# Kernel tuning notes

Hardware: AMD Instinct MI355X
Metric: run time of the kernel (lower is better)

Reference implementation:

```python
import jax, jax.numpy as jnp
import numpy as np
import math

EMBED_DIM = 1024
WINDOW = 512


def setup_inputs() -> dict:
    key = jax.random.key(0)
    k_x, k_mb, k_wg, k_bg = jax.random.split(key, 4)
    x = jax.random.normal(k_x, (4, 4096, EMBED_DIM), dtype=jnp.float32)
    memory_bank = jax.random.normal(k_mb, (WINDOW, EMBED_DIM), dtype=jnp.float32)
    # memory_gate: nn.Linear(embed_dim, embed_dim)
    lim = 1.0 / math.sqrt(EMBED_DIM)
    gate_w = jax.random.uniform(k_wg, (EMBED_DIM, EMBED_DIM), jnp.float32, -lim, lim)
    gate_b = jax.random.uniform(k_bg, (EMBED_DIM,), jnp.float32, -lim, lim)
    return {"x": x, "memory_bank": memory_bank, "gate_w": gate_w, "gate_b": gate_b}


def reference(x, memory_bank, gate_w, gate_b):
    d = x.shape[-1]
    # attention scores over fixed memory bank: [B, S, W]
    scores = jnp.einsum("bsd,wd->bsw", x, memory_bank) / jnp.sqrt(jnp.asarray(d, x.dtype))
    attn = jax.nn.softmax(scores, axis=-1)
    retrieved = jnp.einsum("bsw,wd->bsd", attn, memory_bank)
    gate = jax.nn.sigmoid(jnp.einsum("bsd,ed->bse", x, gate_w) + gate_b)
    return gate * x + (1.0 - gate) * retrieved
```

## Files before the change

kernel.cpp:

```cpp
#include <hip/hip_runtime.h>
#include <hip/hip_bf16.h>

#define EMBED 1024
#define WINDOW 512
#define NROWS 16384

typedef __attribute__((ext_vector_type(4))) float f32x4;
typedef __bf16 bf16x8 __attribute__((ext_vector_type(8)));

#define GLDS(g, l)                                                        \
  __builtin_amdgcn_global_load_lds(                                       \
      (const __attribute__((address_space(1))) void*)(const void*)(g),    \
      (__attribute__((address_space(3))) void*)(void*)(l), 16, 0, 0)

__global__ __launch_bounds__(256) void cast_bf16_kernel(
    const float* __restrict__ in, __bf16* __restrict__ out, int n8) {
  int i = blockIdx.x * blockDim.x + threadIdx.x;
  if (i >= n8) return;
  const f32x4* p = (const f32x4*)(in + (size_t)i * 8);
  f32x4 a = p[0], b = p[1];
  bf16x8 o = {(__bf16)a[0], (__bf16)a[1], (__bf16)a[2], (__bf16)a[3],
              (__bf16)b[0], (__bf16)b[1], (__bf16)b[2], (__bf16)b[3]};
  *(bf16x8*)(out + (size_t)i * 8) = o;
}

__global__ __launch_bounds__(256) void transpose_mb_kernel(
    const float* __restrict__ mb, __bf16* __restrict__ mbt) {
  int idx = blockIdx.x * blockDim.x + threadIdx.x;
  int w = idx >> 10, d = idx & 1023;
  mbt[(size_t)d * WINDOW + w] = (__bf16)mb[idx];
}

__global__ __launch_bounds__(256) void softmax_kernel(__bf16* __restrict__ s1) {
  const int row = blockIdx.x * 4 + (threadIdx.x >> 6);
  const int lane = threadIdx.x & 63;
  __bf16* p = s1 + (size_t)row * WINDOW + lane * 8;
  bf16x8 v = *(const bf16x8*)p;
  float f[8];
  float mx = -1e30f;
#pragma unroll
  for (int j = 0; j < 8; ++j) {
    f[j] = (float)v[j] * 0.03125f;
    mx = fmaxf(mx, f[j]);
  }
#pragma unroll
  for (int off = 1; off < 64; off <<= 1) mx = fmaxf(mx, __shfl_xor(mx, off));
  float s = 0.f;
#pragma unroll
  for (int j = 0; j < 8; ++j) {
    f[j] = __expf(f[j] - mx);
    s += f[j];
  }
#pragma unroll
  for (int off = 1; off < 64; off <<= 1) s += __shfl_xor(s, off);
  const float inv = 1.0f / s;
  bf16x8 o;
#pragma unroll
  for (int j = 0; j < 8; ++j) o[j] = (__bf16)(f[j] * inv);
  *(bf16x8*)p = o;
}

#define SLOADFRAGS(cb, kk)                                                    \
  {                                                                           \
    const __bf16* As_ = &ldsA[cb][(warp_m * 64 + fr) * 64];                   \
    const __bf16* Bs_ = &ldsB[cb][(warp_n * 64 + fr) * 64];                   \
    const int pg_ = (((kk)*4 + fq) ^ (fr & 7)) * 8;                           \
    _Pragma("unroll") for (int m = 0; m < 4; ++m)                             \
        af[m] = *(const bf16x8*)(As_ + m * 16 * 64 + pg_);                    \
    _Pragma("unroll") for (int n = 0; n < 4; ++n)                             \
        bfv[n] = *(const bf16x8*)(Bs_ + n * 16 * 64 + pg_);                   \
  }

#define SMFMA16(ACC)                                                          \
  {                                                                           \
    __builtin_amdgcn_s_barrier();                                             \
    asm volatile("s_waitcnt lgkmcnt(0)" ::: "memory");                        \
    __builtin_amdgcn_s_setprio(1);                                            \
    _Pragma("unroll") for (int m = 0; m < 4; ++m)                             \
        _Pragma("unroll") for (int n = 0; n < 4; ++n)                         \
            ACC[m][n] = __builtin_amdgcn_mfma_f32_16x16x32_bf16(              \
                af[m], bfv[n], ACC[m][n], 0, 0, 0);                           \
    __builtin_amdgcn_s_setprio(0);                                            \
    __builtin_amdgcn_s_barrier();                                             \
  }

__global__ __launch_bounds__(512, 2) void gemm_scores_kernel(
    const __bf16* __restrict__ xb, const __bf16* __restrict__ mbb,
    __bf16* __restrict__ s1) {
  __shared__ __align__(16) __bf16 ldsA[3][256 * 64];
  __shared__ __align__(16) __bf16 ldsB[3][128 * 64];
  const int tid = threadIdx.x;
  const int lane = tid & 63;
  const int wave = tid >> 6;
  const int bid = blockIdx.x;
  const int xcd = bid & 7;
  const int idx = bid >> 3;
  const int bm = xcd * 8 + (idx & 7);
  const int bn = idx >> 3;
  const int row0 = bm * 256;
  const int col0 = bn * 128;
  const int warp_m = wave >> 1;
  const int warp_n = wave & 1;
  const int srow = lane >> 3;
  const int sgc = (lane & 7) ^ srow;
  const int wv32 = wave * 32;
  const int wv16 = wave * 16;
  const int fr = lane & 15;
  const int fq = lane >> 4;

  const __bf16* aS = xb + (size_t)(row0 + wv32 + srow) * EMBED + sgc * 8;
  const __bf16* bS = mbb + (size_t)(col0 + wv16 + srow) * EMBED + sgc * 8;

#define STAGE_S1(vt, buf)                                                     \
  {                                                                           \
    const int k0_ = (vt)*64;                                                  \
    _Pragma("unroll") for (int c = 0; c < 2; ++c)                             \
        GLDS(aS + (size_t)c * 8 * EMBED + k0_, &ldsA[buf][(wv32 + c * 8) * 64]); \
    GLDS(bS + k0_, &ldsB[buf][wv16 * 64]);                                    \
  }
#define STAGE_S2(vt, buf)                                                     \
  {                                                                           \
    const int k0_ = (vt)*64;                                                  \
    _Pragma("unroll") for (int c = 2; c < 4; ++c)                             \
        GLDS(aS + (size_t)c * 8 * EMBED + k0_, &ldsA[buf][(wv32 + c * 8) * 64]); \
    GLDS(bS + (size_t)8 * EMBED + k0_, &ldsB[buf][(wv16 + 8) * 64]);          \
  }

  f32x4 acc[4][4];
#pragma unroll
  for (int m = 0; m < 4; ++m)
#pragma unroll
    for (int n = 0; n < 4; ++n) acc[m][n] = (f32x4){0.f, 0.f, 0.f, 0.f};
  bf16x8 af[4], bfv[4];

  STAGE_S1(0, 0); STAGE_S2(0, 0);
  STAGE_S1(1, 1); STAGE_S2(1, 1);
  asm volatile("s_waitcnt vmcnt(6)" ::: "memory");
  __builtin_amdgcn_s_barrier();

  const int NT = 16;
  for (int vt = 0; vt < NT; ++vt) {
    const int cb = vt % 3;
    const int nb = (vt + 2) % 3;
    SLOADFRAGS(cb, 0);
    if (vt + 2 < NT) STAGE_S1(vt + 2, nb);
    SMFMA16(acc);
    SLOADFRAGS(cb, 1);
    if (vt + 2 < NT) STAGE_S2(vt + 2, nb);
    if (vt < NT - 2) {
      asm volatile("s_waitcnt vmcnt(6)" ::: "memory");
    } else if (vt == NT - 2) {
      asm volatile("s_waitcnt vmcnt(0)" ::: "memory");
    }
    SMFMA16(acc);
  }
#undef STAGE_S1
#undef STAGE_S2

#pragma unroll
  for (int n = 0; n < 4; ++n) {
    const int col = col0 + warp_n * 64 + n * 16 + fr;
#pragma unroll
    for (int m = 0; m < 4; ++m)
#pragma unroll
      for (int j = 0; j < 4; ++j) {
        const int row = row0 + warp_m * 64 + m * 16 + fq * 4 + j;
        s1[(size_t)row * WINDOW + col] = (__bf16)acc[m][n][j];
      }
  }
}

__global__ __launch_bounds__(256, 2) void dual_fused128_kernel(
    const __bf16* __restrict__ s1, const __bf16* __restrict__ xb,
    const __bf16* __restrict__ mbt, const __bf16* __restrict__ gwb,
    const float* __restrict__ gb, float* __restrict__ out) {
  __shared__ __align__(16) __bf16 ldsA[2][128 * 64];
  __shared__ __align__(16) __bf16 ldsB[2][128 * 64];
  const int tid = threadIdx.x, lane = tid & 63, wave = tid >> 6;
  const int bid = blockIdx.x;
  const int xcd = bid & 7;
  const int g = bid >> 3;
  const int bm = xcd * 16 + (g & 15);
  const int bn = g >> 4;
  const int row0 = bm * 128, col0 = bn * 128;
  const int warp_m = wave >> 1, warp_n = wave & 1;
  const int fr = lane & 15, fq = lane >> 4;
  const int srow = lane >> 3;
  const int sgc = (lane & 7) ^ srow;
  const int wv32 = wave * 32;

  const __bf16* aR = s1 + (size_t)(row0 + wv32 + srow) * WINDOW + sgc * 8;
  const __bf16* bR = mbt + (size_t)(col0 + wv32 + srow) * WINDOW + sgc * 8;
  const __bf16* aG = xb + (size_t)(row0 + wv32 + srow) * EMBED + sgc * 8;
  const __bf16* bG = gwb + (size_t)(col0 + wv32 + srow) * EMBED + sgc * 8;

#define STG(vt, buf)                                                          \
  {                                                                           \
    if ((vt) < 8) {                                                           \
      const int k0_ = (vt)*64;                                                \
      _Pragma("unroll") for (int c = 0; c < 4; ++c)                           \
          GLDS(aR + (size_t)c * 8 * WINDOW + k0_,                             \
               &ldsA[buf][(wv32 + c * 8) * 64]);                              \
      _Pragma("unroll") for (int c = 0; c < 4; ++c)                           \
          GLDS(bR + (size_t)c * 8 * WINDOW + k0_,                             \
               &ldsB[buf][(wv32 + c * 8) * 64]);                              \
    } else {                                                                  \
      const int k0_ = ((vt)-8) * 64;                                          \
      _Pragma("unroll") for (int c = 0; c < 4; ++c)                           \
          GLDS(aG + (size_t)c * 8 * EMBED + k0_,                              \
               &ldsA[buf][(wv32 + c * 8) * 64]);                              \
      _Pragma("unroll") for (int c = 0; c < 4; ++c)                           \
          GLDS(bG + (size_t)c * 8 * EMBED + k0_,                              \
               &ldsB[buf][(wv32 + c * 8) * 64]);                              \
    }                                                                         \
  }

#define BARF                                                                  \
  {                                                                           \
    asm volatile("" ::: "memory");                                            \
    __builtin_amdgcn_s_barrier();                                             \
    asm volatile("" ::: "memory");                                            \
  }

#define COMPUTE(ACC, cur)                                                     \
  {                                                                           \
    const __bf16* As_ = &ldsA[cur][(warp_m * 64 + fr) * 64];                  \
    const __bf16* Bs_ = &ldsB[cur][(warp_n * 64 + fr) * 64];                  \
    _Pragma("unroll") for (int kk = 0; kk < 2; ++kk) {                        \
      const int pg_ = ((kk * 4 + fq) ^ (fr & 7)) * 8;                         \
      bf16x8 af[4], bfv[4];                                                   \
      _Pragma("unroll") for (int m = 0; m < 4; ++m)                           \
          af[m] = *(const bf16x8*)(As_ + m * 16 * 64 + pg_);                  \
      _Pragma("unroll") for (int n = 0; n < 4; ++n)                           \
          bfv[n] = *(const bf16x8*)(Bs_ + n * 16 * 64 + pg_);                 \
      __builtin_amdgcn_s_setprio(1);                                          \
      _Pragma("unroll") for (int m = 0; m < 4; ++m)                           \
          _Pragma("unroll") for (int n = 0; n < 4; ++n)                       \
              ACC[m][n] = __builtin_amdgcn_mfma_f32_16x16x32_bf16(            \
                  af[m], bfv[n], ACC[m][n], 0, 0, 0);                         \
      __builtin_amdgcn_s_setprio(0);                                          \
    }                                                                         \
  }

  f32x4 accr[4][4], accg[4][4];
#pragma unroll
  for (int m = 0; m < 4; ++m)
#pragma unroll
    for (int n = 0; n < 4; ++n) {
      accr[m][n] = (f32x4){0.f, 0.f, 0.f, 0.f};
      accg[m][n] = (f32x4){0.f, 0.f, 0.f, 0.f};
    }

  STG(0, 0);
  for (int vt = 0; vt < 8; ++vt) {
    const int cur = vt & 1;
    STG(vt + 1, cur ^ 1);
    asm volatile("s_waitcnt vmcnt(8)" ::: "memory");
    BARF;
    COMPUTE(accr, cur);
    BARF;
  }
  for (int vt = 8; vt < 24; ++vt) {
    const int cur = vt & 1;
    if (vt + 1 < 24) {
      STG(vt + 1, cur ^ 1);
      asm volatile("s_waitcnt vmcnt(8)" ::: "memory");
    } else {
      asm volatile("s_waitcnt vmcnt(0)" ::: "memory");
    }
    BARF;
    COMPUTE(accg, cur);
    BARF;
  }
#undef STG
#undef COMPUTE
#undef BARF

#pragma unroll
  for (int n = 0; n < 4; ++n) {
    const int col = col0 + warp_n * 64 + n * 16 + fr;
    const float bias = gb[col];
#pragma unroll
    for (int m = 0; m < 4; ++m) {
#pragma unroll
      for (int j = 0; j < 4; ++j) {
        const int row = row0 + warp_m * 64 + m * 16 + fq * 4 + j;
        const size_t o = (size_t)row * EMBED + col;
        const float gt = 1.0f / (1.0f + __expf(-(accg[m][n][j] + bias)));
        const float xv = (float)xb[o];
        out[o] = gt * xv + (1.0f - gt) * accr[m][n][j];
      }
    }
  }
}

extern "C" void kernel_launch(void* const* d_in, const int* in_sizes, int n_in,
                              void* d_out, int out_size, void* d_ws,
                              size_t ws_size, hipStream_t stream) {
  const float* x = (const float*)d_in[0];
  const float* mb = (const float*)d_in[1];
  const float* gw = (const float*)d_in[2];
  const float* gb = (const float*)d_in[3];
  float* out = (float*)d_out;

  char* ws = (char*)d_ws;
  __bf16* xb = (__bf16*)(ws);
  __bf16* mbb = (__bf16*)(ws + 33554432);
  __bf16* mbt = (__bf16*)(ws + 34603008);
  __bf16* gwb = (__bf16*)(ws + 35651584);
  __bf16* s1 = (__bf16*)(ws + 37748736);

  cast_bf16_kernel<<<8192, 256, 0, stream>>>(x, xb, 2097152);
  cast_bf16_kernel<<<256, 256, 0, stream>>>(mb, mbb, 65536);
  cast_bf16_kernel<<<512, 256, 0, stream>>>(gw, gwb, 131072);
  transpose_mb_kernel<<<2048, 256, 0, stream>>>(mb, mbt);
  gemm_scores_kernel<<<256, 512, 0, stream>>>(xb, mbb, s1);
  softmax_kernel<<<4096, 256, 0, stream>>>(s1);
  dual_fused128_kernel<<<1024, 256, 0, stream>>>(s1, xb, mbt, gwb, gb, out);
}
```

Measured before the change: 124.4 us.

## Enlarge dual GEMM tile to 256x256 and pack retrieved accumulator to bf16

The fused retrieval+gate GEMM moves from 128x128 tiles with 256 threads to 256x256 tiles with 512 threads, launching 256 blocks instead of 1024. Each wave now computes a 128x64 sub-tile, reusing B fragments across two A halves to raise arithmetic intensity and cut global/LDS traffic per FLOP. To keep register pressure manageable, the retrieved-value accumulator is packed to bf16 before the gate GEMM starts. This adds rounding to the retrieved term and raises LDS use per block (128KB), which lowers occupancy to about one block per CU.

```diff
diff --git a/kernel.cpp b/kernel.cpp
--- a/kernel.cpp
+++ b/kernel.cpp
@@ -170,20 +170,19 @@
   }
 }
 
-__global__ __launch_bounds__(256, 2) void dual_fused128_kernel(
+__global__ __launch_bounds__(512, 2) void dual_fused256_kernel(
     const __bf16* __restrict__ s1, const __bf16* __restrict__ xb,
     const __bf16* __restrict__ mbt, const __bf16* __restrict__ gwb,
     const float* __restrict__ gb, float* __restrict__ out) {
-  __shared__ __align__(16) __bf16 ldsA[2][128 * 64];
-  __shared__ __align__(16) __bf16 ldsB[2][128 * 64];
+  __shared__ __align__(16) __bf16 ldsA[2][256 * 64];
+  __shared__ __align__(16) __bf16 ldsB[2][256 * 64];
   const int tid = threadIdx.x, lane = tid & 63, wave = tid >> 6;
   const int bid = blockIdx.x;
-  const int xcd = bid & 7;
-  const int g = bid >> 3;
-  const int bm = xcd * 16 + (g & 15);
-  const int bn = g >> 4;
-  const int row0 = bm * 128, col0 = bn * 128;
-  const int warp_m = wave >> 1, warp_n = wave & 1;
+  const int bm = (bid & 7) * 8 + ((bid >> 3) & 7);
+  const int bn = bid >> 6;
+  const int row0 = bm * 256, col0 = bn * 256;
+  const int warp_m = wave >> 2;
+  const int warp_n = wave & 3;
   const int fr = lane & 15, fq = lane >> 4;
   const int srow = lane >> 3;
   const int sgc = (lane & 7) ^ srow;
@@ -224,32 +223,37 @@
 
 #define COMPUTE(ACC, cur)                                                     \
   {                                                                           \
-    const __bf16* As_ = &ldsA[cur][(warp_m * 64 + fr) * 64];                  \
+    const __bf16* As_ = &ldsA[cur][(warp_m * 128 + fr) * 64];                 \
     const __bf16* Bs_ = &ldsB[cur][(warp_n * 64 + fr) * 64];                  \
     _Pragma("unroll") for (int kk = 0; kk < 2; ++kk) {                        \
       const int pg_ = ((kk * 4 + fq) ^ (fr & 7)) * 8;                         \
       bf16x8 af[4], bfv[4];                                                   \
+      _Pragma("unroll") for (int n = 0; n < 4; ++n)                           \
+          bfv[n] = *(const bf16x8*)(Bs_ + n * 16 * 64 + pg_);                 \
       _Pragma("unroll") for (int m = 0; m < 4; ++m)                           \
           af[m] = *(const bf16x8*)(As_ + m * 16 * 64 + pg_);                  \
-      _Pragma("unroll") for (int n = 0; n < 4; ++n)                           \
-          bfv[n] = *(const bf16x8*)(Bs_ + n * 16 * 64 + pg_);                 \
       __builtin_amdgcn_s_setprio(1);                                          \
       _Pragma("unroll") for (int m = 0; m < 4; ++m)                           \
           _Pragma("unroll") for (int n = 0; n < 4; ++n)                       \
               ACC[m][n] = __builtin_amdgcn_mfma_f32_16x16x32_bf16(            \
                   af[m], bfv[n], ACC[m][n], 0, 0, 0);                         \
       __builtin_amdgcn_s_setprio(0);                                          \
+      _Pragma("unroll") for (int m = 0; m < 4; ++m)                           \
+          af[m] = *(const bf16x8*)(As_ + (64 + m * 16) * 64 + pg_);           \
+      __builtin_amdgcn_s_setprio(1);                                          \
+      _Pragma("unroll") for (int m = 0; m < 4; ++m)                           \
+          _Pragma("unroll") for (int n = 0; n < 4; ++n)                       \
+              ACC[4 + m][n] = __builtin_amdgcn_mfma_f32_16x16x32_bf16(        \
+                  af[m], bfv[n], ACC[4 + m][n], 0, 0, 0);                     \
+      __builtin_amdgcn_s_setprio(0);                                          \
     }                                                                         \
   }
 
-  f32x4 accr[4][4], accg[4][4];
-#pragma unroll
-  for (int m = 0; m < 4; ++m)
-#pragma unroll
-    for (int n = 0; n < 4; ++n) {
-      accr[m][n] = (f32x4){0.f, 0.f, 0.f, 0.f};
-      accg[m][n] = (f32x4){0.f, 0.f, 0.f, 0.f};
-    }
+  f32x4 accr[8][4];
+#pragma unroll
+  for (int m = 0; m < 8; ++m)
+#pragma unroll
+    for (int n = 0; n < 4; ++n) accr[m][n] = (f32x4){0.f, 0.f, 0.f, 0.f};
 
   STG(0, 0);
   for (int vt = 0; vt < 8; ++vt) {
@@ -260,6 +264,26 @@
     COMPUTE(accr, cur);
     BARF;
   }
+
+  unsigned pk[8][4][2];
+#pragma unroll
+  for (int m = 0; m < 8; ++m)
+#pragma unroll
+    for (int n = 0; n < 4; ++n) {
+      unsigned b0 = (unsigned)__builtin_bit_cast(unsigned short, (__bf16)accr[m][n][0]);
+      unsigned b1 = (unsigned)__builtin_bit_cast(unsigned short, (__bf16)accr[m][n][1]);
+      unsigned b2 = (unsigned)__builtin_bit_cast(unsigned short, (__bf16)accr[m][n][2]);
+      unsigned b3 = (unsigned)__builtin_bit_cast(unsigned short, (__bf16)accr[m][n][3]);
+      pk[m][n][0] = (b1 << 16) | b0;
+      pk[m][n][1] = (b3 << 16) | b2;
+    }
+
+  f32x4 accg[8][4];
+#pragma unroll
+  for (int m = 0; m < 8; ++m)
+#pragma unroll
+    for (int n = 0; n < 4; ++n) accg[m][n] = (f32x4){0.f, 0.f, 0.f, 0.f};
+
   for (int vt = 8; vt < 24; ++vt) {
     const int cur = vt & 1;
     if (vt + 1 < 24) {
@@ -281,14 +305,19 @@
     const int col = col0 + warp_n * 64 + n * 16 + fr;
     const float bias = gb[col];
 #pragma unroll
-    for (int m = 0; m < 4; ++m) {
+    for (int m = 0; m < 8; ++m) {
+      float rv[4];
+      rv[0] = __builtin_bit_cast(float, pk[m][n][0] << 16);
+      rv[1] = __builtin_bit_cast(float, pk[m][n][0] & 0xffff0000u);
+      rv[2] = __builtin_bit_cast(float, pk[m][n][1] << 16);
+      rv[3] = __builtin_bit_cast(float, pk[m][n][1] & 0xffff0000u);
 #pragma unroll
       for (int j = 0; j < 4; ++j) {
-        const int row = row0 + warp_m * 64 + m * 16 + fq * 4 + j;
+        const int row = row0 + warp_m * 128 + m * 16 + fq * 4 + j;
         const size_t o = (size_t)row * EMBED + col;
-        const float gt = 1.0f / (1.0f + __expf(-(accg[m][n][j] + bias)));
+        const float g = 1.0f / (1.0f + __expf(-(accg[m][n][j] + bias)));
         const float xv = (float)xb[o];
-        out[o] = gt * xv + (1.0f - gt) * accr[m][n][j];
+        out[o] = g * xv + (1.0f - g) * rv[j];
       }
     }
   }
@@ -316,5 +345,5 @@
   transpose_mb_kernel<<<2048, 256, 0, stream>>>(mb, mbt);
   gemm_scores_kernel<<<256, 512, 0, stream>>>(xb, mbb, s1);
   softmax_kernel<<<4096, 256, 0, stream>>>(s1);
-  dual_fused128_kernel<<<1024, 256, 0, stream>>>(s1, xb, mbt, gwb, gb, out);
-}
+  dual_fused256_kernel<<<256, 512, 0, stream>>>(s1, xb, mbt, gwb, gb, out);
+}
```

Measured after the change: 165.6 us. +33.1%, slower.

## Switch dual GEMM to BK=32 with four-stage LDS pipeline

Applied to the files above, without the earlier changes.

Halves the K tile of the fused retrieval/gate GEMM from 64 to 32 and moves from double buffering to a 4-slot ring with three tiles in flight. The LDS swizzle and load mapping are changed to match the narrower tile. The goal is to hide more global-load latency behind MFMA work. In exchange there are twice as many barrier pairs per K, less MFMA work per barrier, and an explicit lgkmcnt wait before the MFMAs.

```diff
diff --git a/kernel.cpp b/kernel.cpp
--- a/kernel.cpp
+++ b/kernel.cpp
@@ -170,12 +170,12 @@
   }
 }
 
-__global__ __launch_bounds__(256, 2) void dual_fused128_kernel(
+__global__ __launch_bounds__(256, 2) void dual_bk32_kernel(
     const __bf16* __restrict__ s1, const __bf16* __restrict__ xb,
     const __bf16* __restrict__ mbt, const __bf16* __restrict__ gwb,
     const float* __restrict__ gb, float* __restrict__ out) {
-  __shared__ __align__(16) __bf16 ldsA[2][128 * 64];
-  __shared__ __align__(16) __bf16 ldsB[2][128 * 64];
+  __shared__ __align__(16) __bf16 ldsA[4][128 * 32];
+  __shared__ __align__(16) __bf16 ldsB[4][128 * 32];
   const int tid = threadIdx.x, lane = tid & 63, wave = tid >> 6;
   const int bid = blockIdx.x;
   const int xcd = bid & 7;
@@ -185,8 +185,8 @@
   const int row0 = bm * 128, col0 = bn * 128;
   const int warp_m = wave >> 1, warp_n = wave & 1;
   const int fr = lane & 15, fq = lane >> 4;
-  const int srow = lane >> 3;
-  const int sgc = (lane & 7) ^ srow;
+  const int srow = lane >> 2;
+  const int sgc = (lane & 3) ^ (srow & 3);
   const int wv32 = wave * 32;
 
   const __bf16* aR = s1 + (size_t)(row0 + wv32 + srow) * WINDOW + sgc * 8;
@@ -194,24 +194,20 @@
   const __bf16* aG = xb + (size_t)(row0 + wv32 + srow) * EMBED + sgc * 8;
   const __bf16* bG = gwb + (size_t)(col0 + wv32 + srow) * EMBED + sgc * 8;
 
-#define STG(vt, buf)                                                          \
-  {                                                                           \
-    if ((vt) < 8) {                                                           \
-      const int k0_ = (vt)*64;                                                \
-      _Pragma("unroll") for (int c = 0; c < 4; ++c)                           \
-          GLDS(aR + (size_t)c * 8 * WINDOW + k0_,                             \
-               &ldsA[buf][(wv32 + c * 8) * 64]);                              \
-      _Pragma("unroll") for (int c = 0; c < 4; ++c)                           \
-          GLDS(bR + (size_t)c * 8 * WINDOW + k0_,                             \
-               &ldsB[buf][(wv32 + c * 8) * 64]);                              \
+#define STG(vt, slot)                                                         \
+  {                                                                           \
+    if ((vt) < 16) {                                                          \
+      const int k0_ = (vt)*32;                                                \
+      GLDS(aR + k0_, &ldsA[slot][wv32 * 32]);                                 \
+      GLDS(aR + (size_t)16 * WINDOW + k0_, &ldsA[slot][(wv32 + 16) * 32]);    \
+      GLDS(bR + k0_, &ldsB[slot][wv32 * 32]);                                 \
+      GLDS(bR + (size_t)16 * WINDOW + k0_, &ldsB[slot][(wv32 + 16) * 32]);    \
     } else {                                                                  \
-      const int k0_ = ((vt)-8) * 64;                                          \
-      _Pragma("unroll") for (int c = 0; c < 4; ++c)                           \
-          GLDS(aG + (size_t)c * 8 * EMBED + k0_,                              \
-               &ldsA[buf][(wv32 + c * 8) * 64]);                              \
-      _Pragma("unroll") for (int c = 0; c < 4; ++c)                           \
-          GLDS(bG + (size_t)c * 8 * EMBED + k0_,                              \
-               &ldsB[buf][(wv32 + c * 8) * 64]);                              \
+      const int k0_ = ((vt)-16) * 32;                                         \
+      GLDS(aG + k0_, &ldsA[slot][wv32 * 32]);                                 \
+      GLDS(aG + (size_t)16 * EMBED + k0_, &ldsA[slot][(wv32 + 16) * 32]);     \
+      GLDS(bG + k0_, &ldsB[slot][wv32 * 32]);                                 \
+      GLDS(bG + (size_t)16 * EMBED + k0_, &ldsB[slot][(wv32 + 16) * 32]);     \
     }                                                                         \
   }
 
@@ -222,24 +218,23 @@
     asm volatile("" ::: "memory");                                            \
   }
 
-#define COMPUTE(ACC, cur)                                                     \
-  {                                                                           \
-    const __bf16* As_ = &ldsA[cur][(warp_m * 64 + fr) * 64];                  \
-    const __bf16* Bs_ = &ldsB[cur][(warp_n * 64 + fr) * 64];                  \
-    _Pragma("unroll") for (int kk = 0; kk < 2; ++kk) {                        \
-      const int pg_ = ((kk * 4 + fq) ^ (fr & 7)) * 8;                         \
-      bf16x8 af[4], bfv[4];                                                   \
-      _Pragma("unroll") for (int m = 0; m < 4; ++m)                           \
-          af[m] = *(const bf16x8*)(As_ + m * 16 * 64 + pg_);                  \
-      _Pragma("unroll") for (int n = 0; n < 4; ++n)                           \
-          bfv[n] = *(const bf16x8*)(Bs_ + n * 16 * 64 + pg_);                 \
-      __builtin_amdgcn_s_setprio(1);                                          \
-      _Pragma("unroll") for (int m = 0; m < 4; ++m)                           \
-          _Pragma("unroll") for (int n = 0; n < 4; ++n)                       \
-              ACC[m][n] = __builtin_amdgcn_mfma_f32_16x16x32_bf16(            \
-                  af[m], bfv[n], ACC[m][n], 0, 0, 0);                         \
-      __builtin_amdgcn_s_setprio(0);                                          \
-    }                                                                         \
+#define COMPUTE(ACC, slot)                                                    \
+  {                                                                           \
+    const __bf16* As_ = &ldsA[slot][(warp_m * 64 + fr) * 32];                 \
+    const __bf16* Bs_ = &ldsB[slot][(warp_n * 64 + fr) * 32];                 \
+    const int pg_ = (fq ^ (fr & 3)) * 8;                                      \
+    bf16x8 af[4], bfv[4];                                                     \
+    _Pragma("unroll") for (int m = 0; m < 4; ++m)                             \
+        af[m] = *(const bf16x8*)(As_ + m * 16 * 32 + pg_);                    \
+    _Pragma("unroll") for (int n = 0; n < 4; ++n)                             \
+        bfv[n] = *(const bf16x8*)(Bs_ + n * 16 * 32 + pg_);                   \
+    asm volatile("s_waitcnt lgkmcnt(0)" ::: "memory");                        \
+    __builtin_amdgcn_s_setprio(1);                                            \
+    _Pragma("unroll") for (int m = 0; m < 4; ++m)                             \
+        _Pragma("unroll") for (int n = 0; n < 4; ++n)                         \
+            ACC[m][n] = __builtin_amdgcn_mfma_f32_16x16x32_bf16(              \
+                af[m], bfv[n], ACC[m][n], 0, 0, 0);                           \
+    __builtin_amdgcn_s_setprio(0);                                            \
   }
 
   f32x4 accr[4][4], accg[4][4];
@@ -251,25 +246,25 @@
       accg[m][n] = (f32x4){0.f, 0.f, 0.f, 0.f};
     }
 
-  STG(0, 0);
-  for (int vt = 0; vt < 8; ++vt) {
-    const int cur = vt & 1;
-    STG(vt + 1, cur ^ 1);
-    asm volatile("s_waitcnt vmcnt(8)" ::: "memory");
-    BARF;
-    COMPUTE(accr, cur);
-    BARF;
-  }
-  for (int vt = 8; vt < 24; ++vt) {
-    const int cur = vt & 1;
-    if (vt + 1 < 24) {
-      STG(vt + 1, cur ^ 1);
+  const int NT = 48;
+  STG(0, 0); STG(1, 1); STG(2, 2);
+
+  for (int vt = 0; vt < NT; ++vt) {
+    const int slot = vt & 3;
+    if (vt < NT - 2) {
       asm volatile("s_waitcnt vmcnt(8)" ::: "memory");
+    } else if (vt == NT - 2) {
+      asm volatile("s_waitcnt vmcnt(4)" ::: "memory");
     } else {
       asm volatile("s_waitcnt vmcnt(0)" ::: "memory");
     }
     BARF;
-    COMPUTE(accg, cur);
+    if (vt + 3 < NT) STG(vt + 3, (vt + 3) & 3);
+    if (vt < 16) {
+      COMPUTE(accr, slot);
+    } else {
+      COMPUTE(accg, slot);
+    }
     BARF;
   }
 #undef STG
@@ -316,5 +311,5 @@
   transpose_mb_kernel<<<2048, 256, 0, stream>>>(mb, mbt);
   gemm_scores_kernel<<<256, 512, 0, stream>>>(xb, mbb, s1);
   softmax_kernel<<<4096, 256, 0, stream>>>(s1);
-  dual_fused128_kernel<<<1024, 256, 0, stream>>>(s1, xb, mbt, gwb, gb, out);
-}
+  dual_bk32_kernel<<<1024, 256, 0, stream>>>(s1, xb, mbt, gwb, gb, out);
+}
```

New measurement: 152.3 us. 1.22x slower.

## Fuse x cast, scores GEMM and softmax into one full-row kernel

Applied to the files above, without the earlier changes.

Replaces the separate x-to-bf16 cast, the scores GEMM and the softmax kernel with one kernel. Each 512-thread block handles 64 rows across all 512 window columns, so it can do the whole row softmax in registers and shared memory. It reads fp32 x directly, converts it on the fly, and writes both the LDS tile and the bf16 xb copy that the later kernel uses. This drops two launches and a round trip of the score matrix through global memory. In exchange the tile is smaller (64 rows, K step 32) and the buffering is only double, and the block-index mapping of the dual fused kernel is also reordered.

```diff
diff --git a/kernel.cpp b/kernel.cpp
--- a/kernel.cpp
+++ b/kernel.cpp
@@ -31,99 +31,68 @@
   mbt[(size_t)d * WINDOW + w] = (__bf16)mb[idx];
 }
 
-__global__ __launch_bounds__(256) void softmax_kernel(__bf16* __restrict__ s1) {
-  const int row = blockIdx.x * 4 + (threadIdx.x >> 6);
-  const int lane = threadIdx.x & 63;
-  __bf16* p = s1 + (size_t)row * WINDOW + lane * 8;
-  bf16x8 v = *(const bf16x8*)p;
-  float f[8];
-  float mx = -1e30f;
-#pragma unroll
-  for (int j = 0; j < 8; ++j) {
-    f[j] = (float)v[j] * 0.03125f;
-    mx = fmaxf(mx, f[j]);
-  }
-#pragma unroll
-  for (int off = 1; off < 64; off <<= 1) mx = fmaxf(mx, __shfl_xor(mx, off));
-  float s = 0.f;
-#pragma unroll
-  for (int j = 0; j < 8; ++j) {
-    f[j] = __expf(f[j] - mx);
-    s += f[j];
-  }
-#pragma unroll
-  for (int off = 1; off < 64; off <<= 1) s += __shfl_xor(s, off);
-  const float inv = 1.0f / s;
-  bf16x8 o;
-#pragma unroll
-  for (int j = 0; j < 8; ++j) o[j] = (__bf16)(f[j] * inv);
-  *(bf16x8*)p = o;
-}
-
-#define SLOADFRAGS(cb, kk)                                                    \
-  {                                                                           \
-    const __bf16* As_ = &ldsA[cb][(warp_m * 64 + fr) * 64];                   \
-    const __bf16* Bs_ = &ldsB[cb][(warp_n * 64 + fr) * 64];                   \
-    const int pg_ = (((kk)*4 + fq) ^ (fr & 7)) * 8;                           \
+__global__ __launch_bounds__(512, 2) void scores_mega_kernel(
+    const float* __restrict__ x, const __bf16* __restrict__ mbb,
+    __bf16* __restrict__ xb, __bf16* __restrict__ s1) {
+  __shared__ __align__(16) __bf16 ldsA[2][64 * 32];
+  __shared__ __align__(16) __bf16 ldsB[2][512 * 32];
+  __shared__ float sred[8][64];
+  __shared__ float sfin[64];
+  const int tid = threadIdx.x, lane = tid & 63, wave = tid >> 6;
+  const int row0 = blockIdx.x * 64;
+  const int warp_n = wave;
+  const int fr = lane & 15, fq = lane >> 4;
+
+  const int arow = tid >> 3;
+  const int acol4 = (tid & 7) * 4;
+  const int ag = (tid >> 1) & 3;
+  const int ah = tid & 1;
+  const int fA = (arow & 3) ^ ((arow >> 2) & 3);
+  const int aws = arow * 32 + ((ag ^ fA) * 8) + ah * 4;
+  const float* aSrc = x + (size_t)(row0 + arow) * EMBED + acol4;
+  __bf16* xbDst = xb + (size_t)(row0 + arow) * EMBED + acol4;
+
+  const int srow = lane >> 2;
+  const int sgc = (lane & 3) ^ ((lane >> 2) & 3) ^ ((lane >> 4) & 3);
+  const __bf16* bSrc = mbb + (size_t)(wave * 64 + srow) * EMBED + sgc * 8;
+
+#define STG_B(t, buf)                                                         \
+  {                                                                           \
+    _Pragma("unroll") for (int c = 0; c < 4; ++c)                             \
+        GLDS(bSrc + (size_t)c * 16 * EMBED + (t) * 32,                        \
+             &ldsB[buf][(wave * 64 + c * 16) * 32]);                          \
+  }
+
+#define PACK_WRITE(av, buf, t)                                                \
+  {                                                                           \
+    unsigned u0 =                                                             \
+        ((unsigned)__builtin_bit_cast(unsigned short, (__bf16)av[1]) << 16) | \
+        (unsigned)__builtin_bit_cast(unsigned short, (__bf16)av[0]);          \
+    unsigned u1 =                                                             \
+        ((unsigned)__builtin_bit_cast(unsigned short, (__bf16)av[3]) << 16) | \
+        (unsigned)__builtin_bit_cast(unsigned short, (__bf16)av[2]);          \
+    uint2 w2 = {u0, u1};                                                      \
+    *(uint2*)(&ldsA[buf][aws]) = w2;                                          \
+    *(uint2*)(xbDst + (t) * 32) = w2;                                         \
+  }
+
+#define MCOMPUTE(cur)                                                         \
+  {                                                                           \
+    const __bf16* As_ = &ldsA[cur][0];                                        \
+    const __bf16* Bs_ = &ldsB[cur][(warp_n * 64) * 32];                       \
+    const int pg_ = (fq ^ ((fr & 3) ^ ((fr >> 2) & 3))) * 8;                  \
+    bf16x8 af[4], bfv[4];                                                     \
     _Pragma("unroll") for (int m = 0; m < 4; ++m)                             \
-        af[m] = *(const bf16x8*)(As_ + m * 16 * 64 + pg_);                    \
+        af[m] = *(const bf16x8*)(As_ + (m * 16 + fr) * 32 + pg_);             \
     _Pragma("unroll") for (int n = 0; n < 4; ++n)                             \
-        bfv[n] = *(const bf16x8*)(Bs_ + n * 16 * 64 + pg_);                   \
-  }
-
-#define SMFMA16(ACC)                                                          \
-  {                                                                           \
-    __builtin_amdgcn_s_barrier();                                             \
+        bfv[n] = *(const bf16x8*)(Bs_ + (n * 16 + fr) * 32 + pg_);            \
     asm volatile("s_waitcnt lgkmcnt(0)" ::: "memory");                        \
     __builtin_amdgcn_s_setprio(1);                                            \
     _Pragma("unroll") for (int m = 0; m < 4; ++m)                             \
         _Pragma("unroll") for (int n = 0; n < 4; ++n)                         \
-            ACC[m][n] = __builtin_amdgcn_mfma_f32_16x16x32_bf16(              \
-                af[m], bfv[n], ACC[m][n], 0, 0, 0);                           \
+            acc[m][n] = __builtin_amdgcn_mfma_f32_16x16x32_bf16(              \
+                af[m], bfv[n], acc[m][n], 0, 0, 0);                           \
     __builtin_amdgcn_s_setprio(0);                                            \
-    __builtin_amdgcn_s_barrier();                                             \
-  }
-
-__global__ __launch_bounds__(512, 2) void gemm_scores_kernel(
-    const __bf16* __restrict__ xb, const __bf16* __restrict__ mbb,
-    __bf16* __restrict__ s1) {
-  __shared__ __align__(16) __bf16 ldsA[3][256 * 64];
-  __shared__ __align__(16) __bf16 ldsB[3][128 * 64];
-  const int tid = threadIdx.x;
-  const int lane = tid & 63;
-  const int wave = tid >> 6;
-  const int bid = blockIdx.x;
-  const int xcd = bid & 7;
-  const int idx = bid >> 3;
-  const int bm = xcd * 8 + (idx & 7);
-  const int bn = idx >> 3;
-  const int row0 = bm * 256;
-  const int col0 = bn * 128;
-  const int warp_m = wave >> 1;
-  const int warp_n = wave & 1;
-  const int srow = lane >> 3;
-  const int sgc = (lane & 7) ^ srow;
-  const int wv32 = wave * 32;
-  const int wv16 = wave * 16;
-  const int fr = lane & 15;
-  const int fq = lane >> 4;
-
-  const __bf16* aS = xb + (size_t)(row0 + wv32 + srow) * EMBED + sgc * 8;
-  const __bf16* bS = mbb + (size_t)(col0 + wv16 + srow) * EMBED + sgc * 8;
-
-#define STAGE_S1(vt, buf)                                                     \
-  {                                                                           \
-    const int k0_ = (vt)*64;                                                  \
-    _Pragma("unroll") for (int c = 0; c < 2; ++c)                             \
-        GLDS(aS + (size_t)c * 8 * EMBED + k0_, &ldsA[buf][(wv32 + c * 8) * 64]); \
-    GLDS(bS + k0_, &ldsB[buf][wv16 * 64]);                                    \
-  }
-#define STAGE_S2(vt, buf)                                                     \
-  {                                                                           \
-    const int k0_ = (vt)*64;                                                  \
-    _Pragma("unroll") for (int c = 2; c < 4; ++c)                             \
-        GLDS(aS + (size_t)c * 8 * EMBED + k0_, &ldsA[buf][(wv32 + c * 8) * 64]); \
-    GLDS(bS + (size_t)8 * EMBED + k0_, &ldsB[buf][(wv16 + 8) * 64]);          \
   }
 
   f32x4 acc[4][4];
@@ -131,43 +100,121 @@
   for (int m = 0; m < 4; ++m)
 #pragma unroll
     for (int n = 0; n < 4; ++n) acc[m][n] = (f32x4){0.f, 0.f, 0.f, 0.f};
-  bf16x8 af[4], bfv[4];
-
-  STAGE_S1(0, 0); STAGE_S2(0, 0);
-  STAGE_S1(1, 1); STAGE_S2(1, 1);
-  asm volatile("s_waitcnt vmcnt(6)" ::: "memory");
-  __builtin_amdgcn_s_barrier();
-
-  const int NT = 16;
-  for (int vt = 0; vt < NT; ++vt) {
-    const int cb = vt % 3;
-    const int nb = (vt + 2) % 3;
-    SLOADFRAGS(cb, 0);
-    if (vt + 2 < NT) STAGE_S1(vt + 2, nb);
-    SMFMA16(acc);
-    SLOADFRAGS(cb, 1);
-    if (vt + 2 < NT) STAGE_S2(vt + 2, nb);
-    if (vt < NT - 2) {
-      asm volatile("s_waitcnt vmcnt(6)" ::: "memory");
-    } else if (vt == NT - 2) {
+
+  {
+    f32x4 a0 = *(const f32x4*)(aSrc);
+    asm volatile("" ::: "memory");
+    STG_B(0, 0);
+    asm volatile("s_waitcnt vmcnt(0)" ::: "memory");
+    PACK_WRITE(a0, 0, 0);
+    asm volatile("s_waitcnt lgkmcnt(0)" ::: "memory");
+    __builtin_amdgcn_s_barrier();
+  }
+
+  for (int t = 0; t < 32; ++t) {
+    const int cur = t & 1;
+    f32x4 an;
+    if (t + 1 < 32) {
+      an = *(const f32x4*)(aSrc + (t + 1) * 32);
+      asm volatile("" ::: "memory");
+      STG_B(t + 1, cur ^ 1);
+    }
+    MCOMPUTE(cur);
+    if (t + 1 < 32) {
+      asm volatile("s_waitcnt vmcnt(4)" ::: "memory");
+      PACK_WRITE(an, cur ^ 1, t + 1);
       asm volatile("s_waitcnt vmcnt(0)" ::: "memory");
-    }
-    SMFMA16(acc);
-  }
-#undef STAGE_S1
-#undef STAGE_S2
-
-#pragma unroll
-  for (int n = 0; n < 4; ++n) {
-    const int col = col0 + warp_n * 64 + n * 16 + fr;
+      asm volatile("s_waitcnt lgkmcnt(0)" ::: "memory");
+    }
+    __builtin_amdgcn_s_barrier();
+  }
+#undef STG_B
+#undef PACK_WRITE
+#undef MCOMPUTE
+
+  const float scale = 0.03125f;
+  float rmx[4][4];
+#pragma unroll
+  for (int m = 0; m < 4; ++m)
+#pragma unroll
+    for (int j = 0; j < 4; ++j) {
+      float v = -1e30f;
+#pragma unroll
+      for (int n = 0; n < 4; ++n) {
+        acc[m][n][j] *= scale;
+        v = fmaxf(v, acc[m][n][j]);
+      }
+      rmx[m][j] = v;
+    }
+#pragma unroll
+  for (int off = 1; off < 16; off <<= 1)
 #pragma unroll
     for (int m = 0; m < 4; ++m)
 #pragma unroll
-      for (int j = 0; j < 4; ++j) {
-        const int row = row0 + warp_m * 64 + m * 16 + fq * 4 + j;
-        s1[(size_t)row * WINDOW + col] = (__bf16)acc[m][n][j];
+      for (int j = 0; j < 4; ++j)
+        rmx[m][j] = fmaxf(rmx[m][j], __shfl_xor(rmx[m][j], off));
+  if (fr == 0) {
+#pragma unroll
+    for (int m = 0; m < 4; ++m)
+#pragma unroll
+      for (int j = 0; j < 4; ++j) sred[warp_n][m * 16 + fq * 4 + j] = rmx[m][j];
+  }
+  __syncthreads();
+  if (tid < 64) {
+    float v = sred[0][tid];
+#pragma unroll
+    for (int w = 1; w < 8; ++w) v = fmaxf(v, sred[w][tid]);
+    sfin[tid] = v;
+  }
+  __syncthreads();
+
+  float rsm[4][4];
+#pragma unroll
+  for (int m = 0; m < 4; ++m)
+#pragma unroll
+    for (int j = 0; j < 4; ++j) {
+      const float fm = sfin[m * 16 + fq * 4 + j];
+      float s = 0.f;
+#pragma unroll
+      for (int n = 0; n < 4; ++n) {
+        float e = __expf(acc[m][n][j] - fm);
+        acc[m][n][j] = e;
+        s += e;
       }
-  }
+      rsm[m][j] = s;
+    }
+#pragma unroll
+  for (int off = 1; off < 16; off <<= 1)
+#pragma unroll
+    for (int m = 0; m < 4; ++m)
+#pragma unroll
+      for (int j = 0; j < 4; ++j) rsm[m][j] += __shfl_xor(rsm[m][j], off);
+  if (fr == 0) {
+#pragma unroll
+    for (int m = 0; m < 4; ++m)
+#pragma unroll
+      for (int j = 0; j < 4; ++j) sred[warp_n][m * 16 + fq * 4 + j] = rsm[m][j];
+  }
+  __syncthreads();
+  if (tid < 64) {
+    float v = sred[0][tid];
+#pragma unroll
+    for (int w = 1; w < 8; ++w) v += sred[w][tid];
+    sfin[tid] = 1.0f / v;
+  }
+  __syncthreads();
+
+#pragma unroll
+  for (int m = 0; m < 4; ++m)
+#pragma unroll
+    for (int j = 0; j < 4; ++j) {
+      const int row = row0 + m * 16 + fq * 4 + j;
+      const float inv = sfin[m * 16 + fq * 4 + j];
+#pragma unroll
+      for (int n = 0; n < 4; ++n)
+        s1[(size_t)row * WINDOW + warp_n * 64 + n * 16 + fr] =
+            (__bf16)(acc[m][n][j] * inv);
+    }
 }
 
 __global__ __launch_bounds__(256, 2) void dual_fused128_kernel(
@@ -180,8 +227,8 @@
   const int bid = blockIdx.x;
   const int xcd = bid & 7;
   const int g = bid >> 3;
-  const int bm = xcd * 16 + (g & 15);
-  const int bn = g >> 4;
+  const int bm = xcd * 16 + (g >> 3);
+  const int bn = g & 7;
   const int row0 = bm * 128, col0 = bn * 128;
   const int warp_m = wave >> 1, warp_n = wave & 1;
   const int fr = lane & 15, fq = lane >> 4;
@@ -310,11 +357,9 @@
   __bf16* gwb = (__bf16*)(ws + 35651584);
   __bf16* s1 = (__bf16*)(ws + 37748736);
 
-  cast_bf16_kernel<<<8192, 256, 0, stream>>>(x, xb, 2097152);
   cast_bf16_kernel<<<256, 256, 0, stream>>>(mb, mbb, 65536);
   cast_bf16_kernel<<<512, 256, 0, stream>>>(gw, gwb, 131072);
   transpose_mb_kernel<<<2048, 256, 0, stream>>>(mb, mbt);
-  gemm_scores_kernel<<<256, 512, 0, stream>>>(xb, mbb, s1);
-  softmax_kernel<<<4096, 256, 0, stream>>>(s1);
+  scores_mega_kernel<<<256, 512, 0, stream>>>(x, mbb, xb, s1);
   dual_fused128_kernel<<<1024, 256, 0, stream>>>(s1, xb, mbt, gwb, gb, out);
 }
```

New measurement: 125.4 us. No clear change (+0.8%).
